# Performance work log

Measured on AMD Instinct MI355X. Metric: run time of the kernel, lower is better.

Reference implementation:

```python
import jax, jax.numpy as jnp
import numpy as np

DIM = 1024
NUM_HEADS = 16
DIM_HEAD = 64
INNER = NUM_HEADS * DIM_HEAD  # 1024
SCALE = DIM_HEAD ** -0.5


def setup_inputs() -> dict:
    key = jax.random.key(0)
    ks = jax.random.split(key, 8)
    B, SQ, SK = 2, 2048, 4096
    x = jax.random.normal(ks[0], (B, SQ, DIM), dtype=jnp.float32)
    context = jax.random.normal(ks[1], (B, SK, DIM), dtype=jnp.float32)
    # LayerNorm params
    ln_gamma = jnp.ones((DIM,), jnp.float32)
    ln_beta = jnp.zeros((DIM,), jnp.float32)
    # Linear weights, stored as [in, out] so y = x @ W (torch Linear weight transposed)
    w_q = jax.random.normal(ks[2], (DIM, INNER), dtype=jnp.float32) / np.sqrt(DIM)
    w_kv = jax.random.normal(ks[3], (DIM, 2 * INNER), dtype=jnp.float32) / np.sqrt(DIM)
    w_out = jax.random.normal(ks[4], (INNER, DIM), dtype=jnp.float32) / np.sqrt(INNER)
    b_out = jnp.zeros((DIM,), jnp.float32)
    # torch init is 0.0 (tanh(0)=0); use a nonzero value so output/grads are nontrivial
    gate = jnp.array([0.5], jnp.float32)
    return {"x": x, "context": context, "ln_gamma": ln_gamma, "ln_beta": ln_beta,
            "w_q": w_q, "w_kv": w_kv, "w_out": w_out, "b_out": b_out, "gate": gate}


def _layernorm(x, gamma, beta, eps=1e-5):
    mu = jnp.mean(x, axis=-1, keepdims=True)
    var = jnp.mean(jnp.square(x - mu), axis=-1, keepdims=True)
    return (x - mu) * jax.lax.rsqrt(var + eps) * gamma + beta


def reference(x, context, ln_gamma, ln_beta, w_q, w_kv, w_out, b_out, gate):
    B, SQ, _ = x.shape
    SK = context.shape[1]
    xn = _layernorm(x, ln_gamma, ln_beta)
    q = (xn @ w_q).reshape(B, SQ, NUM_HEADS, DIM_HEAD)
    kv = context @ w_kv
    k, v = jnp.split(kv, 2, axis=-1)
    k = k.reshape(B, SK, NUM_HEADS, DIM_HEAD)
    v = v.reshape(B, SK, NUM_HEADS, DIM_HEAD)
    # scores: [B, H, SQ, SK]
    scores = jnp.einsum('bqhd,bkhd->bhqk', q * SCALE, k)
    attn = jax.nn.softmax(scores, axis=-1)
    out = jnp.einsum('bhqk,bkhd->bqhd', attn, v).reshape(B, SQ, INNER)
    out = out @ w_out + b_out
    return out * jnp.tanh(gate[0])
```

## Files before the change

kernel.cpp:

```cpp
#include <hip/hip_runtime.h>
#include <hip/hip_bf16.h>
#include <stdint.h>

#define DIMM  1024
#define NHEAD 16
#define DHEAD 64
#define BB    2
#define SQL   2048
#define SKL   4096
#define KVW   2048

typedef __attribute__((ext_vector_type(8))) short short8;
typedef __attribute__((ext_vector_type(4))) float f32x4;
typedef __attribute__((ext_vector_type(4))) unsigned short us4;

typedef const __attribute__((address_space(1))) uint32_t gu32_t;
typedef __attribute__((address_space(3))) uint32_t lu32_t;

#define GLDS16(gp, lp) __builtin_amdgcn_global_load_lds((gu32_t*)(gp), (lu32_t*)(lp), 16, 0, 0)

static __device__ __forceinline__ unsigned short f2bf(float f) {
  union { float f; uint32_t u; } v; v.f = f;
  uint32_t r = v.u + 0x7fffu + ((v.u >> 16) & 1u);
  return (unsigned short)(r >> 16);
}

__global__ __launch_bounds__(256) void k_transpose_cast(const float* __restrict__ in,
                                                        unsigned short* __restrict__ out,
                                                        int K, int N) {
  __shared__ float tile[32][33];
  int n0 = blockIdx.x * 32, k0 = blockIdx.y * 32;
  int tx = threadIdx.x, ty = threadIdx.y;
  #pragma unroll
  for (int i = 0; i < 4; i++)
    tile[ty + i * 8][tx] = in[(size_t)(k0 + ty + i * 8) * N + n0 + tx];
  __syncthreads();
  #pragma unroll
  for (int i = 0; i < 4; i++)
    out[(size_t)(n0 + ty + i * 8) * K + k0 + tx] = f2bf(tile[tx][ty + i * 8]);
}

__global__ __launch_bounds__(256) void k_cast(const float* __restrict__ in,
                                              unsigned short* __restrict__ out) {
  size_t i = (size_t)(blockIdx.x * 256 + threadIdx.x) * 4;
  float4 v = *(const float4*)(in + i);
  us4 o;
  o.x = f2bf(v.x); o.y = f2bf(v.y); o.z = f2bf(v.z); o.w = f2bf(v.w);
  *(us4*)(out + i) = o;
}

__global__ __launch_bounds__(256) void k_ln(const float* __restrict__ x,
                                            const float* __restrict__ gamma,
                                            const float* __restrict__ beta,
                                            unsigned short* __restrict__ out) {
  const int row = blockIdx.x, tid = threadIdx.x;
  const float* xr = x + (size_t)row * DIMM;
  float4 v = *(const float4*)(xr + tid * 4);
  float s = v.x + v.y + v.z + v.w;
  float ss = v.x * v.x + v.y * v.y + v.z * v.z + v.w * v.w;
  #pragma unroll
  for (int m = 1; m < 64; m <<= 1) {
    s += __shfl_xor(s, m);
    ss += __shfl_xor(ss, m);
  }
  __shared__ float red[8];
  const int wid = tid >> 6, lane = tid & 63;
  if (lane == 0) { red[wid] = s; red[4 + wid] = ss; }
  __syncthreads();
  s = red[0] + red[1] + red[2] + red[3];
  ss = red[4] + red[5] + red[6] + red[7];
  float mu = s * (1.0f / DIMM);
  float var = ss * (1.0f / DIMM) - mu * mu;
  float rstd = rsqrtf(var + 1e-5f);
  float4 g = *(const float4*)(gamma + tid * 4);
  float4 bt = *(const float4*)(beta + tid * 4);
  us4 o;
  o.x = f2bf((v.x - mu) * rstd * g.x + bt.x);
  o.y = f2bf((v.y - mu) * rstd * g.y + bt.y);
  o.z = f2bf((v.z - mu) * rstd * g.z + bt.z);
  o.w = f2bf((v.w - mu) * rstd * g.w + bt.w);
  *(us4*)(out + (size_t)row * DIMM + tid * 4) = o;
}

template<int MODE>
__global__ __launch_bounds__(256) void k_gemm_bt(const unsigned short* __restrict__ A,
                                                 const unsigned short* __restrict__ BT,
                                                 void* __restrict__ Cv,
                                                 int M, int N, int K,
                                                 const float* __restrict__ bias,
                                                 const float* __restrict__ gate) {
  __shared__ unsigned short lA[2][128 * 32];
  __shared__ unsigned short lB[2][128 * 32];
  const int tid = threadIdx.x;
  const int wid = tid >> 6, lane = tid & 63;
  const int kg = lane >> 4, lr = lane & 15;
  const int wr = wid >> 1, wc = wid & 1;
  const int im = blockIdx.x, in_ = blockIdx.y;
  const int nt = K >> 5;
  const size_t baseA = (size_t)im * 128 * K;
  const size_t baseB = (size_t)in_ * 128 * K;

  f32x4 acc[4][4];
  #pragma unroll
  for (int m = 0; m < 4; m++)
    #pragma unroll
    for (int n = 0; n < 4; n++) {
      f32x4 z = {0.0f, 0.0f, 0.0f, 0.0f};
      acc[m][n] = z;
    }

  auto GSTAGE = [&](int bufi, int t) {
    int k0 = t << 5;
    #pragma unroll
    for (int j = 0; j < 2; j++) {
      int e = wid * 1024 + j * 512 + lane * 8;
      int row = e >> 5;
      int g = (e >> 3) & 3;
      int col = (g ^ ((row >> 1) & 3)) << 3;
      GLDS16(A + baseA + (size_t)row * K + k0 + col, &lA[bufi][e]);
      GLDS16(BT + baseB + (size_t)row * K + k0 + col, &lB[bufi][e]);
    }
  };

  GSTAGE(0, 0);
  __syncthreads();
  int buf = 0;
  for (int t = 0; t < nt; t++) {
    if (t + 1 < nt) GSTAGE(buf ^ 1, t + 1);
    short8 a[4], b[4];
    #pragma unroll
    for (int m = 0; m < 4; m++) {
      int row = wr * 64 + m * 16 + lr;
      a[m] = *(const short8*)&lA[buf][row * 32 + ((kg ^ ((row >> 1) & 3)) << 3)];
    }
    #pragma unroll
    for (int n = 0; n < 4; n++) {
      int row = wc * 64 + n * 16 + lr;
      b[n] = *(const short8*)&lB[buf][row * 32 + ((kg ^ ((row >> 1) & 3)) << 3)];
    }
    #pragma unroll
    for (int m = 0; m < 4; m++)
      #pragma unroll
      for (int n = 0; n < 4; n++)
        acc[m][n] = __builtin_amdgcn_mfma_f32_16x16x32_bf16(a[m], b[n], acc[m][n], 0, 0, 0);
    __syncthreads();
    buf ^= 1;
  }

  const int r0 = im * 128 + wr * 64;
  const int c0 = in_ * 128 + wc * 64;
  if constexpr (MODE == 0) {
    unsigned short* C = (unsigned short*)Cv;
    #pragma unroll
    for (int m = 0; m < 4; m++)
      #pragma unroll
      for (int n = 0; n < 4; n++)
        #pragma unroll
        for (int j = 0; j < 4; j++)
          C[(size_t)(r0 + m * 16 + kg * 4 + j) * N + c0 + n * 16 + lr] = f2bf(acc[m][n][j]);
  } else {
    float* C = (float*)Cv;
    float gl = tanhf(gate[0]);
    #pragma unroll
    for (int m = 0; m < 4; m++)
      #pragma unroll
      for (int n = 0; n < 4; n++)
        #pragma unroll
        for (int j = 0; j < 4; j++) {
          int col = c0 + n * 16 + lr;
          C[(size_t)(r0 + m * 16 + kg * 4 + j) * N + col] = (acc[m][n][j] + bias[col]) * gl;
        }
  }
}

__global__ __launch_bounds__(256, 2) void k_attn(const unsigned short* __restrict__ Q,
                                                 const unsigned short* __restrict__ KV,
                                                 unsigned short* __restrict__ O) {
  __shared__ unsigned short sK[2][64 * 64];
  __shared__ unsigned short sV[2][64 * 64];
  __shared__ unsigned short sP[4][2][16 * 72];

  const int tid = threadIdx.x;
  const int wid = tid >> 6, lane = tid & 63;
  const int kg = lane >> 4, lr = lane & 15;
  const int qb = blockIdx.x, bh = blockIdx.y;
  const int b = bh >> 4, h = bh & 15;

  const unsigned short* Qp = Q + (size_t)b * SQL * DIMM + h * DHEAD;
  const unsigned short* Kp = KV + (size_t)b * SKL * KVW + h * DHEAD;
  const unsigned short* Vp = Kp + DIMM;

  const int qr0 = qb * 128 + wid * 32;

  short8 qa[2][2];
  #pragma unroll
  for (int m = 0; m < 2; m++)
    #pragma unroll
    for (int ks = 0; ks < 2; ks++) {
      short8 v = *(const short8*)(Qp + (size_t)(qr0 + m * 16 + lr) * DIMM + ks * 32 + kg * 8);
      #pragma unroll
      for (int j = 0; j < 8; j++) {
        union { float f; uint32_t u; } c;
        c.u = ((uint32_t)(unsigned short)v[j]) << 16;
        v[j] = (short)f2bf(c.f * 0.1803368801111f);
      }
      qa[m][ks] = v;
    }

  f32x4 oacc[2][4];
  #pragma unroll
  for (int m = 0; m < 2; m++)
    #pragma unroll
    for (int n = 0; n < 4; n++) {
      f32x4 z = {0.0f, 0.0f, 0.0f, 0.0f};
      oacc[m][n] = z;
    }
  float rs[2] = {0.0f, 0.0f};

  const unsigned short* ksrc[2]; int kdst[2];
  #pragma unroll
  for (int j = 0; j < 2; j++) {
    int e = wid * 1024 + j * 512 + lane * 8;
    int row = e >> 6;
    int col = (((e >> 3) & 7) ^ (row & 7)) << 3;
    ksrc[j] = Kp + (size_t)row * KVW + col;
    kdst[j] = e;
  }
  const unsigned short* vsrc[2]; int vdst[2];
  #pragma unroll
  for (int j = 0; j < 2; j++) {
    int g = tid + j * 256;
    int key = (g >> 5) * 4 + ((g & 7) >> 1);
    int d0v = ((g >> 3) & 3) * 16 + (g & 1) * 8;
    vsrc[j] = Vp + (size_t)key * KVW + d0v;
    vdst[j] = g * 8;
  }

  auto STAGE = [&](int bufi, int kt) {
    size_t off = (size_t)kt * 64 * KVW;
    #pragma unroll
    for (int j = 0; j < 2; j++) GLDS16(ksrc[j] + off, &sK[bufi][kdst[j]]);
    #pragma unroll
    for (int j = 0; j < 2; j++) GLDS16(vsrc[j] + off, &sV[bufi][vdst[j]]);
  };

  uint32_t sVbase[2];
  sVbase[0] = (uint32_t)(size_t)(lu32_t*)&sV[0][0] + (uint32_t)(kg * 1024 + lr * 8);
  sVbase[1] = (uint32_t)(size_t)(lu32_t*)&sV[1][0] + (uint32_t)(kg * 1024 + lr * 8);

  STAGE(0, 0);
  __syncthreads();

  int buf = 0;
  for (int kt = 0; kt < SKL / 64; kt++) {
    const bool more = (kt + 1 < SKL / 64);
    if (more) STAGE(buf ^ 1, kt + 1);

    short8 kb[4][2];
    #pragma unroll
    for (int n = 0; n < 4; n++)
      #pragma unroll
      for (int ks = 0; ks < 2; ks++) {
        int row = n * 16 + lr;
        kb[n][ks] = *(const short8*)&sK[buf][row * 64 + (((ks * 4 + kg) ^ (row & 7)) << 3)];
      }
    f32x4 sc[4][2];
    #pragma unroll
    for (int n = 0; n < 4; n++)
      #pragma unroll
      for (int m = 0; m < 2; m++) {
        f32x4 z = {0.0f, 0.0f, 0.0f, 0.0f};
        sc[n][m] = z;
      }
    #pragma unroll
    for (int n = 0; n < 4; n++)
      #pragma unroll
      for (int m = 0; m < 2; m++)
        #pragma unroll
        for (int ks = 0; ks < 2; ks++)
          sc[n][m] = __builtin_amdgcn_mfma_f32_16x16x32_bf16(kb[n][ks], qa[m][ks], sc[n][m], 0, 0, 0);

    #pragma unroll
    for (int m = 0; m < 2; m++) {
      unsigned short* sPw = &sP[wid][m][0];
      #pragma unroll
      for (int n = 0; n < 4; n++) {
        float p0 = __builtin_amdgcn_exp2f(sc[n][m][0]);
        float p1 = __builtin_amdgcn_exp2f(sc[n][m][1]);
        float p2 = __builtin_amdgcn_exp2f(sc[n][m][2]);
        float p3 = __builtin_amdgcn_exp2f(sc[n][m][3]);
        rs[m] += (p0 + p1) + (p2 + p3);
        uint32_t lo, hi;
        asm("v_cvt_pk_bf16_f32 %0, %1, %2" : "=v"(lo) : "v"(p0), "v"(p1));
        asm("v_cvt_pk_bf16_f32 %0, %1, %2" : "=v"(hi) : "v"(p2), "v"(p3));
        uint2 w2; w2.x = lo; w2.y = hi;
        *(uint2*)&sPw[lr * 72 + n * 16 + kg * 4] = w2;
      }
    }

    asm volatile("" ::: "memory");

    short8 pa[2][2];
    #pragma unroll
    for (int m = 0; m < 2; m++)
      #pragma unroll
      for (int ks2 = 0; ks2 < 2; ks2++)
        pa[m][ks2] = *(const short8*)&sP[wid][m][lr * 72 + ks2 * 32 + kg * 8];

    union { uint4 u; short8 s; } vbu[4][2];
    {
      uint32_t tb = sVbase[buf];
      #pragma unroll
      for (int n = 0; n < 4; n++)
        #pragma unroll
        for (int ks2 = 0; ks2 < 2; ks2++) {
          uint2 t0, t1;
          uint32_t a0 = tb + (uint32_t)(ks2 * 4096 + n * 128);
          asm volatile("ds_read_b64_tr_b16 %0, %1" : "=v"(t0) : "v"(a0));
          asm volatile("ds_read_b64_tr_b16 %0, %1" : "=v"(t1) : "v"(a0 + 512u));
          vbu[n][ks2].u.x = t0.x; vbu[n][ks2].u.y = t0.y;
          vbu[n][ks2].u.z = t1.x; vbu[n][ks2].u.w = t1.y;
        }
    }
    asm volatile("s_waitcnt lgkmcnt(0)" ::: "memory");
    __builtin_amdgcn_sched_barrier(0);

    #pragma unroll
    for (int m = 0; m < 2; m++)
      #pragma unroll
      for (int n = 0; n < 4; n++)
        #pragma unroll
        for (int ks2 = 0; ks2 < 2; ks2++)
          oacc[m][n] = __builtin_amdgcn_mfma_f32_16x16x32_bf16(pa[m][ks2], vbu[n][ks2].s, oacc[m][n], 0, 0, 0);

    __syncthreads();
    buf ^= 1;
  }

  float inv[2];
  #pragma unroll
  for (int m = 0; m < 2; m++) {
    float t = rs[m];
    t += __shfl_xor(t, 16);
    t += __shfl_xor(t, 32);
    inv[m] = 1.0f / t;
  }
  float rq[2][4];
  #pragma unroll
  for (int m = 0; m < 2; m++)
    #pragma unroll
    for (int j = 0; j < 4; j++)
      rq[m][j] = __shfl(inv[m], kg * 4 + j);

  unsigned short* Op = O + (size_t)b * SQL * DIMM + h * DHEAD;
  #pragma unroll
  for (int m = 0; m < 2; m++)
    #pragma unroll
    for (int n = 0; n < 4; n++)
      #pragma unroll
      for (int j = 0; j < 4; j++)
        Op[(size_t)(qr0 + m * 16 + kg * 4 + j) * DIMM + n * 16 + lr] =
            f2bf(oacc[m][n][j] * rq[m][j]);
}

extern "C" void kernel_launch(void* const* d_in, const int* in_sizes, int n_in,
                              void* d_out, int out_size, void* d_ws, size_t ws_size,
                              hipStream_t stream) {
  (void)in_sizes; (void)n_in; (void)out_size; (void)ws_size;
  const float* x     = (const float*)d_in[0];
  const float* ctx   = (const float*)d_in[1];
  const float* gamma = (const float*)d_in[2];
  const float* beta  = (const float*)d_in[3];
  const float* w_q   = (const float*)d_in[4];
  const float* w_kv  = (const float*)d_in[5];
  const float* w_out = (const float*)d_in[6];
  const float* b_out = (const float*)d_in[7];
  const float* gate  = (const float*)d_in[8];
  float* out = (float*)d_out;
  char* ws = (char*)d_ws;

  unsigned short* XN   = (unsigned short*)(ws);
  unsigned short* QB   = (unsigned short*)(ws + (8ull  << 20));
  unsigned short* CTXB = (unsigned short*)(ws + (16ull << 20));
  unsigned short* KVB  = (unsigned short*)(ws + (32ull << 20));
  unsigned short* OB   = (unsigned short*)(ws + (64ull << 20));
  unsigned short* WQT  = (unsigned short*)(ws + (72ull << 20));
  unsigned short* WKVT = (unsigned short*)(ws + (74ull << 20));
  unsigned short* WOT  = (unsigned short*)(ws + (78ull << 20));

  k_transpose_cast<<<dim3(32, 32), dim3(32, 8), 0, stream>>>(w_q, WQT, 1024, 1024);
  k_transpose_cast<<<dim3(64, 32), dim3(32, 8), 0, stream>>>(w_kv, WKVT, 1024, 2048);
  k_transpose_cast<<<dim3(32, 32), dim3(32, 8), 0, stream>>>(w_out, WOT, 1024, 1024);
  k_cast<<<dim3(8192), dim3(256), 0, stream>>>(ctx, CTXB);
  k_ln<<<dim3(4096), dim3(256), 0, stream>>>(x, gamma, beta, XN);
  k_gemm_bt<0><<<dim3(32, 8), dim3(256), 0, stream>>>(XN, WQT, QB, 4096, 1024, 1024, nullptr, nullptr);
  k_gemm_bt<0><<<dim3(64, 16), dim3(256), 0, stream>>>(CTXB, WKVT, KVB, 8192, 2048, 1024, nullptr, nullptr);
  k_attn<<<dim3(16, 32), dim3(256), 0, stream>>>(QB, KVB, OB);
  k_gemm_bt<1><<<dim3(32, 8), dim3(256), 0, stream>>>(OB, WOT, out, 4096, 1024, 1024, b_out, gate);
}
```

Before: 236.6 us.

## Triple-buffer K/V tiles in attention with one barrier per iteration

Moves the K/V shared-memory staging in the attention kernel from a double buffer to a triple buffer, prefetching two tiles ahead. The end-of-iteration __syncthreads is replaced by a vmcnt-counted wait plus a single s_barrier at loop top, and the Q load is issued before the first stages. The goal is to hide more global-load latency and cut one barrier per tile. The cost is 16 KB more LDS per block, which could lower occupancy below two blocks per CU, and the hand-counted vmcnt must stay correct.

Measured after the change: 232.5 us. No clear change (-1.8%).

```diff
diff --git a/kernel.cpp b/kernel.cpp
--- a/kernel.cpp
+++ b/kernel.cpp
@@ -9,6 +9,7 @@
 #define SQL   2048
 #define SKL   4096
 #define KVW   2048
+#define NT    (SKL / 64)
 
 typedef __attribute__((ext_vector_type(8))) short short8;
 typedef __attribute__((ext_vector_type(4))) float f32x4;
@@ -176,8 +177,8 @@
 __global__ __launch_bounds__(256, 2) void k_attn(const unsigned short* __restrict__ Q,
                                                  const unsigned short* __restrict__ KV,
                                                  unsigned short* __restrict__ O) {
-  __shared__ unsigned short sK[2][64 * 64];
-  __shared__ unsigned short sV[2][64 * 64];
+  __shared__ unsigned short sK[3][64 * 64];
+  __shared__ unsigned short sV[3][64 * 64];
   __shared__ unsigned short sP[4][2][16 * 72];
 
   const int tid = threadIdx.x;
@@ -192,12 +193,44 @@
 
   const int qr0 = qb * 128 + wid * 32;
 
+  const unsigned short* ksrc[2]; int kdst[2];
+  #pragma unroll
+  for (int j = 0; j < 2; j++) {
+    int e = wid * 1024 + j * 512 + lane * 8;
+    int row = e >> 6;
+    int col = (((e >> 3) & 7) ^ (row & 7)) << 3;
+    ksrc[j] = Kp + (size_t)row * KVW + col;
+    kdst[j] = e;
+  }
+  const unsigned short* vsrc[2]; int vdst[2];
+  #pragma unroll
+  for (int j = 0; j < 2; j++) {
+    int g = tid + j * 256;
+    int key = (g >> 5) * 4 + ((g & 7) >> 1);
+    int d0v = ((g >> 3) & 3) * 16 + (g & 1) * 8;
+    vsrc[j] = Vp + (size_t)key * KVW + d0v;
+    vdst[j] = g * 8;
+  }
+
+  auto STAGE = [&](int bufi, int kt) {
+    size_t off = (size_t)kt * 64 * KVW;
+    #pragma unroll
+    for (int j = 0; j < 2; j++) GLDS16(ksrc[j] + off, &sK[bufi][kdst[j]]);
+    #pragma unroll
+    for (int j = 0; j < 2; j++) GLDS16(vsrc[j] + off, &sV[bufi][vdst[j]]);
+  };
+
   short8 qa[2][2];
   #pragma unroll
   for (int m = 0; m < 2; m++)
     #pragma unroll
+    for (int ks = 0; ks < 2; ks++)
+      qa[m][ks] = *(const short8*)(Qp + (size_t)(qr0 + m * 16 + lr) * DIMM + ks * 32 + kg * 8);
+  #pragma unroll
+  for (int m = 0; m < 2; m++)
+    #pragma unroll
     for (int ks = 0; ks < 2; ks++) {
-      short8 v = *(const short8*)(Qp + (size_t)(qr0 + m * 16 + lr) * DIMM + ks * 32 + kg * 8);
+      short8 v = qa[m][ks];
       #pragma unroll
       for (int j = 0; j < 8; j++) {
         union { float f; uint32_t u; } c;
@@ -217,44 +250,20 @@
     }
   float rs[2] = {0.0f, 0.0f};
 
-  const unsigned short* ksrc[2]; int kdst[2];
-  #pragma unroll
-  for (int j = 0; j < 2; j++) {
-    int e = wid * 1024 + j * 512 + lane * 8;
-    int row = e >> 6;
-    int col = (((e >> 3) & 7) ^ (row & 7)) << 3;
-    ksrc[j] = Kp + (size_t)row * KVW + col;
-    kdst[j] = e;
-  }
-  const unsigned short* vsrc[2]; int vdst[2];
-  #pragma unroll
-  for (int j = 0; j < 2; j++) {
-    int g = tid + j * 256;
-    int key = (g >> 5) * 4 + ((g & 7) >> 1);
-    int d0v = ((g >> 3) & 3) * 16 + (g & 1) * 8;
-    vsrc[j] = Vp + (size_t)key * KVW + d0v;
-    vdst[j] = g * 8;
-  }
-
-  auto STAGE = [&](int bufi, int kt) {
-    size_t off = (size_t)kt * 64 * KVW;
-    #pragma unroll
-    for (int j = 0; j < 2; j++) GLDS16(ksrc[j] + off, &sK[bufi][kdst[j]]);
-    #pragma unroll
-    for (int j = 0; j < 2; j++) GLDS16(vsrc[j] + off, &sV[bufi][vdst[j]]);
-  };
-
-  uint32_t sVbase[2];
-  sVbase[0] = (uint32_t)(size_t)(lu32_t*)&sV[0][0] + (uint32_t)(kg * 1024 + lr * 8);
-  sVbase[1] = (uint32_t)(size_t)(lu32_t*)&sV[1][0] + (uint32_t)(kg * 1024 + lr * 8);
+  const uint32_t sVb0 = (uint32_t)(size_t)(lu32_t*)&sV[0][0] + (uint32_t)(kg * 1024 + lr * 8);
 
   STAGE(0, 0);
-  __syncthreads();
-
-  int buf = 0;
-  for (int kt = 0; kt < SKL / 64; kt++) {
-    const bool more = (kt + 1 < SKL / 64);
-    if (more) STAGE(buf ^ 1, kt + 1);
+  STAGE(1, 1);
+
+  int cur = 0;
+  for (int kt = 0; kt < NT; kt++) {
+    if (kt < NT - 1) asm volatile("s_waitcnt vmcnt(4)" ::: "memory");
+    else             asm volatile("s_waitcnt vmcnt(0)" ::: "memory");
+    __builtin_amdgcn_s_barrier();
+    if (kt + 2 < NT) {
+      int p2 = cur >= 1 ? cur - 1 : 2;
+      STAGE(p2, kt + 2);
+    }
 
     short8 kb[4][2];
     #pragma unroll
@@ -262,7 +271,7 @@
       #pragma unroll
       for (int ks = 0; ks < 2; ks++) {
         int row = n * 16 + lr;
-        kb[n][ks] = *(const short8*)&sK[buf][row * 64 + (((ks * 4 + kg) ^ (row & 7)) << 3)];
+        kb[n][ks] = *(const short8*)&sK[cur][row * 64 + (((ks * 4 + kg) ^ (row & 7)) << 3)];
       }
     f32x4 sc[4][2];
     #pragma unroll
@@ -309,7 +318,7 @@
 
     union { uint4 u; short8 s; } vbu[4][2];
     {
-      uint32_t tb = sVbase[buf];
+      uint32_t tb = sVb0 + (uint32_t)(cur * 8192);
       #pragma unroll
       for (int n = 0; n < 4; n++)
         #pragma unroll
@@ -333,8 +342,7 @@
         for (int ks2 = 0; ks2 < 2; ks2++)
           oacc[m][n] = __builtin_amdgcn_mfma_f32_16x16x32_bf16(pa[m][ks2], vbu[n][ks2].s, oacc[m][n], 0, 0, 0);
 
-    __syncthreads();
-    buf ^= 1;
+    cur = cur < 2 ? cur + 1 : 0;
   }
 
   float inv[2];
```

## Halve attention query tile per block to raise occupancy, swizzle P in LDS

Applied to the files above, without the earlier changes.

The attention kernel now handles 64 query rows per block (16 per wave) instead of 128, doubling the grid to 1024 blocks and raising launch bounds to 4 blocks per CU. The P staging buffer moves from padded rows to an XOR-swizzled 64-wide layout to avoid LDS bank conflicts with less shared memory. The aim is more waves in flight to hide latency and fewer registers per wave. In exchange, each K/V tile loaded into LDS is reused by half as many query rows, which doubles K/V global traffic and the LDS fill work per output.

Result: no change. 235.8 us (-0.4%).

```diff
diff --git a/kernel.cpp b/kernel.cpp
--- a/kernel.cpp
+++ b/kernel.cpp
@@ -9,6 +9,7 @@
 #define SQL   2048
 #define SKL   4096
 #define KVW   2048
+#define NT    (SKL / 64)
 
 typedef __attribute__((ext_vector_type(8))) short short8;
 typedef __attribute__((ext_vector_type(4))) float f32x4;
@@ -173,12 +174,12 @@
   }
 }
 
-__global__ __launch_bounds__(256, 2) void k_attn(const unsigned short* __restrict__ Q,
+__global__ __launch_bounds__(256, 4) void k_attn(const unsigned short* __restrict__ Q,
                                                  const unsigned short* __restrict__ KV,
                                                  unsigned short* __restrict__ O) {
   __shared__ unsigned short sK[2][64 * 64];
   __shared__ unsigned short sV[2][64 * 64];
-  __shared__ unsigned short sP[4][2][16 * 72];
+  __shared__ unsigned short sP[4][16 * 64];
 
   const int tid = threadIdx.x;
   const int wid = tid >> 6, lane = tid & 63;
@@ -190,32 +191,7 @@
   const unsigned short* Kp = KV + (size_t)b * SKL * KVW + h * DHEAD;
   const unsigned short* Vp = Kp + DIMM;
 
-  const int qr0 = qb * 128 + wid * 32;
-
-  short8 qa[2][2];
-  #pragma unroll
-  for (int m = 0; m < 2; m++)
-    #pragma unroll
-    for (int ks = 0; ks < 2; ks++) {
-      short8 v = *(const short8*)(Qp + (size_t)(qr0 + m * 16 + lr) * DIMM + ks * 32 + kg * 8);
-      #pragma unroll
-      for (int j = 0; j < 8; j++) {
-        union { float f; uint32_t u; } c;
-        c.u = ((uint32_t)(unsigned short)v[j]) << 16;
-        v[j] = (short)f2bf(c.f * 0.1803368801111f);
-      }
-      qa[m][ks] = v;
-    }
-
-  f32x4 oacc[2][4];
-  #pragma unroll
-  for (int m = 0; m < 2; m++)
-    #pragma unroll
-    for (int n = 0; n < 4; n++) {
-      f32x4 z = {0.0f, 0.0f, 0.0f, 0.0f};
-      oacc[m][n] = z;
-    }
-  float rs[2] = {0.0f, 0.0f};
+  const int qr0 = qb * 64 + wid * 16;
 
   const unsigned short* ksrc[2]; int kdst[2];
   #pragma unroll
@@ -244,17 +220,37 @@
     for (int j = 0; j < 2; j++) GLDS16(vsrc[j] + off, &sV[bufi][vdst[j]]);
   };
 
-  uint32_t sVbase[2];
-  sVbase[0] = (uint32_t)(size_t)(lu32_t*)&sV[0][0] + (uint32_t)(kg * 1024 + lr * 8);
-  sVbase[1] = (uint32_t)(size_t)(lu32_t*)&sV[1][0] + (uint32_t)(kg * 1024 + lr * 8);
+  short8 qa[2];
+  #pragma unroll
+  for (int ks = 0; ks < 2; ks++) {
+    short8 v = *(const short8*)(Qp + (size_t)(qr0 + lr) * DIMM + ks * 32 + kg * 8);
+    #pragma unroll
+    for (int j = 0; j < 8; j++) {
+      union { float f; uint32_t u; } c;
+      c.u = ((uint32_t)(unsigned short)v[j]) << 16;
+      v[j] = (short)f2bf(c.f * 0.1803368801111f);
+    }
+    qa[ks] = v;
+  }
+
+  f32x4 oacc[4];
+  #pragma unroll
+  for (int n = 0; n < 4; n++) {
+    f32x4 z = {0.0f, 0.0f, 0.0f, 0.0f};
+    oacc[n] = z;
+  }
+  float rs = 0.0f;
+
+  const uint32_t sVb0 = (uint32_t)(size_t)(lu32_t*)&sV[0][0] + (uint32_t)(kg * 1024 + lr * 8);
+  unsigned char* const sPw = (unsigned char*)&sP[wid][0];
+  const uint32_t swz = (uint32_t)((lr & 7) << 4);
 
   STAGE(0, 0);
   __syncthreads();
 
   int buf = 0;
-  for (int kt = 0; kt < SKL / 64; kt++) {
-    const bool more = (kt + 1 < SKL / 64);
-    if (more) STAGE(buf ^ 1, kt + 1);
+  for (int kt = 0; kt < NT; kt++) {
+    if (kt + 1 < NT) STAGE(buf ^ 1, kt + 1);
 
     short8 kb[4][2];
     #pragma unroll
@@ -264,52 +260,42 @@
         int row = n * 16 + lr;
         kb[n][ks] = *(const short8*)&sK[buf][row * 64 + (((ks * 4 + kg) ^ (row & 7)) << 3)];
       }
-    f32x4 sc[4][2];
+    f32x4 sc[4];
+    #pragma unroll
+    for (int n = 0; n < 4; n++) {
+      f32x4 z = {0.0f, 0.0f, 0.0f, 0.0f};
+      sc[n] = z;
+    }
     #pragma unroll
     for (int n = 0; n < 4; n++)
       #pragma unroll
-      for (int m = 0; m < 2; m++) {
-        f32x4 z = {0.0f, 0.0f, 0.0f, 0.0f};
-        sc[n][m] = z;
-      }
-    #pragma unroll
-    for (int n = 0; n < 4; n++)
-      #pragma unroll
-      for (int m = 0; m < 2; m++)
-        #pragma unroll
-        for (int ks = 0; ks < 2; ks++)
-          sc[n][m] = __builtin_amdgcn_mfma_f32_16x16x32_bf16(kb[n][ks], qa[m][ks], sc[n][m], 0, 0, 0);
-
-    #pragma unroll
-    for (int m = 0; m < 2; m++) {
-      unsigned short* sPw = &sP[wid][m][0];
-      #pragma unroll
-      for (int n = 0; n < 4; n++) {
-        float p0 = __builtin_amdgcn_exp2f(sc[n][m][0]);
-        float p1 = __builtin_amdgcn_exp2f(sc[n][m][1]);
-        float p2 = __builtin_amdgcn_exp2f(sc[n][m][2]);
-        float p3 = __builtin_amdgcn_exp2f(sc[n][m][3]);
-        rs[m] += (p0 + p1) + (p2 + p3);
-        uint32_t lo, hi;
-        asm("v_cvt_pk_bf16_f32 %0, %1, %2" : "=v"(lo) : "v"(p0), "v"(p1));
-        asm("v_cvt_pk_bf16_f32 %0, %1, %2" : "=v"(hi) : "v"(p2), "v"(p3));
-        uint2 w2; w2.x = lo; w2.y = hi;
-        *(uint2*)&sPw[lr * 72 + n * 16 + kg * 4] = w2;
-      }
+      for (int ks = 0; ks < 2; ks++)
+        sc[n] = __builtin_amdgcn_mfma_f32_16x16x32_bf16(kb[n][ks], qa[ks], sc[n], 0, 0, 0);
+
+    #pragma unroll
+    for (int n = 0; n < 4; n++) {
+      float p0 = __builtin_amdgcn_exp2f(sc[n][0]);
+      float p1 = __builtin_amdgcn_exp2f(sc[n][1]);
+      float p2 = __builtin_amdgcn_exp2f(sc[n][2]);
+      float p3 = __builtin_amdgcn_exp2f(sc[n][3]);
+      rs += (p0 + p1) + (p2 + p3);
+      uint32_t lo, hi;
+      asm("v_cvt_pk_bf16_f32 %0, %1, %2" : "=v"(lo) : "v"(p0), "v"(p1));
+      asm("v_cvt_pk_bf16_f32 %0, %1, %2" : "=v"(hi) : "v"(p2), "v"(p3));
+      uint2 w2; w2.x = lo; w2.y = hi;
+      *(uint2*)(sPw + (((uint32_t)(lr * 128 + n * 32 + kg * 8)) ^ swz)) = w2;
     }
 
     asm volatile("" ::: "memory");
 
-    short8 pa[2][2];
-    #pragma unroll
-    for (int m = 0; m < 2; m++)
-      #pragma unroll
-      for (int ks2 = 0; ks2 < 2; ks2++)
-        pa[m][ks2] = *(const short8*)&sP[wid][m][lr * 72 + ks2 * 32 + kg * 8];
+    short8 pa[2];
+    #pragma unroll
+    for (int ks2 = 0; ks2 < 2; ks2++)
+      pa[ks2] = *(const short8*)(sPw + (((uint32_t)(lr * 128 + ks2 * 64 + kg * 16)) ^ swz));
 
     union { uint4 u; short8 s; } vbu[4][2];
     {
-      uint32_t tb = sVbase[buf];
+      uint32_t tb = sVb0 + (uint32_t)(buf * 8192);
       #pragma unroll
       for (int n = 0; n < 4; n++)
         #pragma unroll
@@ -326,41 +312,30 @@
     __builtin_amdgcn_sched_barrier(0);
 
     #pragma unroll
-    for (int m = 0; m < 2; m++)
-      #pragma unroll
-      for (int n = 0; n < 4; n++)
-        #pragma unroll
-        for (int ks2 = 0; ks2 < 2; ks2++)
-          oacc[m][n] = __builtin_amdgcn_mfma_f32_16x16x32_bf16(pa[m][ks2], vbu[n][ks2].s, oacc[m][n], 0, 0, 0);
+    for (int n = 0; n < 4; n++)
+      #pragma unroll
+      for (int ks2 = 0; ks2 < 2; ks2++)
+        oacc[n] = __builtin_amdgcn_mfma_f32_16x16x32_bf16(pa[ks2], vbu[n][ks2].s, oacc[n], 0, 0, 0);
 
     __syncthreads();
     buf ^= 1;
   }
 
-  float inv[2];
-  #pragma unroll
-  for (int m = 0; m < 2; m++) {
-    float t = rs[m];
-    t += __shfl_xor(t, 16);
-    t += __shfl_xor(t, 32);
-    inv[m] = 1.0f / t;
-  }
-  float rq[2][4];
-  #pragma unroll
-  for (int m = 0; m < 2; m++)
+  float t = rs;
+  t += __shfl_xor(t, 16);
+  t += __shfl_xor(t, 32);
+  float inv = 1.0f / t;
+  float rq[4];
+  #pragma unroll
+  for (int j = 0; j < 4; j++)
+    rq[j] = __shfl(inv, kg * 4 + j);
+
+  unsigned short* Op = O + (size_t)b * SQL * DIMM + h * DHEAD;
+  #pragma unroll
+  for (int n = 0; n < 4; n++)
     #pragma unroll
     for (int j = 0; j < 4; j++)
-      rq[m][j] = __shfl(inv[m], kg * 4 + j);
-
-  unsigned short* Op = O + (size_t)b * SQL * DIMM + h * DHEAD;
-  #pragma unroll
-  for (int m = 0; m < 2; m++)
-    #pragma unroll
-    for (int n = 0; n < 4; n++)
-      #pragma unroll
-      for (int j = 0; j < 4; j++)
-        Op[(size_t)(qr0 + m * 16 + kg * 4 + j) * DIMM + n * 16 + lr] =
-            f2bf(oacc[m][n][j] * rq[m][j]);
+      Op[(size_t)(qr0 + kg * 4 + j) * DIMM + n * 16 + lr] = f2bf(oacc[n][j] * rq[j]);
 }
 
 extern "C" void kernel_launch(void* const* d_in, const int* in_sizes, int n_in,
@@ -395,6 +370,6 @@
   k_ln<<<dim3(4096), dim3(256), 0, stream>>>(x, gamma, beta, XN);
   k_gemm_bt<0><<<dim3(32, 8), dim3(256), 0, stream>>>(XN, WQT, QB, 4096, 1024, 1024, nullptr, nullptr);
   k_gemm_bt<0><<<dim3(64, 16), dim3(256), 0, stream>>>(CTXB, WKVT, KVB, 8192, 2048, 1024, nullptr, nullptr);
-  k_attn<<<dim3(16, 32), dim3(256), 0, stream>>>(QB, KVB, OB);
+  k_attn<<<dim3(32, 32), dim3(256), 0, stream>>>(QB, KVB, OB);
   k_gemm_bt<1><<<dim3(32, 8), dim3(256), 0, stream>>>(OB, WOT, out, 4096, 1024, 1024, b_out, gate);
 }
```
